# Performance work log

Hardware: AMD Instinct MI355X
Metric: run time of the kernel (lower is better)

The kernel has to match this reference:

```python
import jax, jax.numpy as jnp
import numpy as np

B, C, N, K = 2, 64, 16384, 16
C_OUT = 64


def setup_inputs() -> dict:
    key = jax.random.key(0)
    k1, k2, k3, k4 = jax.random.split(key, 4)
    x = jax.random.normal(k1, (B, C, N), dtype=jnp.float32)
    edge_index = jax.random.randint(k2, (2, B, N, K), 0, N, dtype=jnp.int64)
    # 1x1 Conv2d params: weight [C_out, 3C], bias [C_out]
    W = jax.random.normal(k3, (C_OUT, 3 * C), dtype=jnp.float32) * (1.0 / np.sqrt(3 * C))
    b = jax.random.normal(k4, (C_OUT,), dtype=jnp.float32) * 0.01
    return {"x": x, "edge_index": edge_index, "W": W, "b": b}


def _gather_nodes(x, idx):
    # x: [B, C, N], idx: [B, N, K] -> [B, C, N, K]
    return jax.vmap(lambda xb, ib: xb[:, ib])(x, idx)


def reference(x, edge_index, W, b):
    # x: [B, C, N]; edge_index: [2, B, N, K]
    x_i = _gather_nodes(x, edge_index[1])          # center features  [B,C,N,K]
    x_j = _gather_nodes(x, edge_index[0])          # neighbor features [B,C,N,K]
    edge_features = x_j - x_i                      # [B,C,N,K]
    global_feature = jnp.mean(x, axis=2, keepdims=True)  # [B,C,1] global mean over nodes
    global_rep = jnp.broadcast_to(global_feature[..., None], x_i.shape)  # [B,C,N,K]
    combined = jnp.concatenate([x_i, edge_features, global_rep], axis=1)  # [B,3C,N,K]
    # BasicConv: 1x1 conv + ReLU (norm=None)
    out = jnp.einsum("bcnk,oc->bonk", combined, W) + b[None, :, None, None]
    out = jax.nn.relu(out)
    return jnp.max(out, axis=-1, keepdims=True)    # [B,C_out,N,1]
```

## Files before the change

### kernel.cpp

```cpp
#include <hip/hip_runtime.h>
#include <hip/hip_bf16.h>


#define NNODES 16384
#define NCH 64

typedef _Float16 half8 __attribute__((ext_vector_type(8)));
typedef float f32x2 __attribute__((ext_vector_type(2)));

__global__ __launch_bounds__(256) void uv_kernel(const float* __restrict__ x,
                                                 const float* __restrict__ W,
                                                 _Float16* __restrict__ u,
                                                 _Float16* __restrict__ v,
                                                 float* __restrict__ g_slots) {
  __shared__ float A[64][64];
  __shared__ float Bm[64][64];
  __shared__ float csum[4][64];
  int t = threadIdx.x;
  {
    int o = t & 63, c0 = (t >> 6) * 16;
    const float* wr = W + o * 192;
#pragma unroll
    for (int i = 0; i < 16; ++i) {
      int c = c0 + i;
      float w1 = wr[c], w2 = wr[64 + c];
      A[c][o] = w1 - w2;
      Bm[c][o] = w2;
    }
  }
  __syncthreads();
  int lane = t & 63;
  int wv = __builtin_amdgcn_readfirstlane(t >> 6);
  int blk = blockIdx.x;
  int b = blk >> 9;
  int mb = (blk & 511) * 32;
  int m0 = mb + wv * 8;
  const float* xb = x + (size_t)b * (NCH * NNODES) + m0;
  f32x2 aU[4], aV[4];
#pragma unroll
  for (int i = 0; i < 4; ++i) {
    aU[i] = (f32x2){0.f, 0.f};
    aV[i] = (f32x2){0.f, 0.f};
  }
#pragma unroll 8
  for (int c = 0; c < 64; ++c) {
    float a = A[c][lane];
    float bb = Bm[c][lane];
    f32x2 a2 = {a, a};
    f32x2 b2 = {bb, bb};
    const float4* xr = (const float4*)(xb + (size_t)c * NNODES);
    float4 q0 = xr[0];
    float4 q1 = xr[1];
    f32x2 p0 = {q0.x, q0.y};
    f32x2 p1 = {q0.z, q0.w};
    f32x2 p2 = {q1.x, q1.y};
    f32x2 p3 = {q1.z, q1.w};
    aU[0] = __builtin_elementwise_fma(a2, p0, aU[0]);
    aU[1] = __builtin_elementwise_fma(a2, p1, aU[1]);
    aU[2] = __builtin_elementwise_fma(a2, p2, aU[2]);
    aU[3] = __builtin_elementwise_fma(a2, p3, aU[3]);
    aV[0] = __builtin_elementwise_fma(b2, p0, aV[0]);
    aV[1] = __builtin_elementwise_fma(b2, p1, aV[1]);
    aV[2] = __builtin_elementwise_fma(b2, p2, aV[2]);
    aV[3] = __builtin_elementwise_fma(b2, p3, aV[3]);
  }
  _Float16* ub = u + ((size_t)b * NNODES + m0) * NCH + lane;
  _Float16* vb = v + ((size_t)b * NNODES + m0) * NCH + lane;
#pragma unroll
  for (int i = 0; i < 4; ++i) {
    ub[(2 * i) * NCH] = (_Float16)aU[i][0];
    ub[(2 * i + 1) * NCH] = (_Float16)aU[i][1];
    vb[(2 * i) * NCH] = (_Float16)aV[i][0];
    vb[(2 * i + 1) * NCH] = (_Float16)aV[i][1];
  }
  {
    int c = t & 63, piece = t >> 6;
    const float4* xr2 =
        (const float4*)(x + (size_t)b * (NCH * NNODES) + (size_t)c * NNODES + mb + piece * 8);
    float4 a0 = xr2[0];
    float4 a1 = xr2[1];
    csum[piece][c] = ((a0.x + a0.y) + (a0.z + a0.w)) + ((a1.x + a1.y) + (a1.z + a1.w));
  }
  __syncthreads();
  if (t < 64) {
    float s = (csum[0][t] + csum[1][t]) + (csum[2][t] + csum[3][t]);
    atomicAdd(&g_slots[((blk & 7) << 7) + b * 64 + t], s);
  }
}

__global__ __launch_bounds__(256) void gather_kernel(const int* __restrict__ ei,
                                                     const _Float16* __restrict__ u,
                                                     const _Float16* __restrict__ v,
                                                     const float* __restrict__ W,
                                                     const float* __restrict__ bias,
                                                     const float* __restrict__ g_slots,
                                                     float* __restrict__ out) {
  __shared__ float tile[64][33];
  __shared__ float gb[64];
  __shared__ float pg[4][64];
  __shared__ float G_s[64];
  int t = threadIdx.x;
  int lane = t & 63;
  int wv = t >> 6;
  int blk = blockIdx.x;
  int xcd = blk & 7;
  int b = xcd >> 2;
  int nb = (blk >> 3) * 4 + (xcd & 3);
  int n0 = nb * 32;
  int q = lane >> 3;
  int r = lane & 7;
  const int* e0b = ei + (size_t)b * NNODES * 16;
  const int* e1b = ei + (size_t)(2 + b) * NNODES * 16;
  int f0 = (n0 + wv * 8) * 16 + q * 16 + r;
  int i0a = e0b[f0];
  int i0b = e0b[f0 + 8];
  int i1a = e1b[f0];
  int i1b = e1b[f0 + 8];
  if (t < 64) {
    float s = 0.f;
#pragma unroll
    for (int sl = 0; sl < 8; ++sl) s += g_slots[sl * 128 + b * 64 + t];
    gb[t] = s * (1.0f / 16384.0f);
  }
  __syncthreads();
  {
    int o = t >> 2, cq = t & 3;
    const float4* wr = (const float4*)(W + o * 192 + 128 + cq * 16);
    const float4* gr = (const float4*)(gb + cq * 16);
    float s = 0.f;
#pragma unroll
    for (int j = 0; j < 4; ++j) {
      float4 w = wr[j];
      float4 gg = gr[j];
      s += w.x * gg.x + w.y * gg.y + w.z * gg.z + w.w * gg.w;
    }
    pg[cq][o] = s;
  }
  __syncthreads();
  if (t < 64) G_s[t] = bias[t] + ((pg[0][t] + pg[1][t]) + (pg[2][t] + pg[3][t]));
  __syncthreads();
  const half8* u8 = (const half8*)(u + (size_t)b * NNODES * NCH) + r;
  const half8* v8 = (const half8*)(v + (size_t)b * NNODES * NCH) + r;
  half8 acc;
#pragma unroll
  for (int j = 0; j < 8; ++j) acc[j] = (_Float16)(-60000.0f);
#pragma unroll
  for (int k = 0; k < 16; ++k) {
    int src = (lane & 56) + (k & 7);
    int m1 = __shfl(k < 8 ? i1a : i1b, src, 64);
    int m0 = __shfl(k < 8 ? i0a : i0b, src, 64);
    half8 a = u8[(size_t)m1 * 8];
    half8 bb = v8[(size_t)m0 * 8];
    half8 s = a + bb;
    acc = __builtin_elementwise_max(acc, s);
  }
  int col = wv * 8 + q;
#pragma unroll
  for (int j = 0; j < 8; ++j) {
    tile[r * 8 + j][col] = fmaxf((float)acc[j] + G_s[r * 8 + j], 0.0f);
  }
  __syncthreads();
#pragma unroll
  for (int j = 0; j < 8; ++j) {
    int o = (t >> 5) + j * 8;
    int c2 = t & 31;
    out[((size_t)b * 64 + o) * NNODES + n0 + c2] = tile[o][c2];
  }
}

extern "C" void kernel_launch(void* const* d_in, const int* in_sizes, int n_in,
                              void* d_out, int out_size, void* d_ws, size_t ws_size,
                              hipStream_t stream) {
  const float* x = (const float*)d_in[0];
  const int* ei = (const int*)d_in[1];
  const float* W = (const float*)d_in[2];
  const float* bias = (const float*)d_in[3];
  float* out = (float*)d_out;

  char* ws = (char*)d_ws;
  _Float16* u = (_Float16*)ws;
  _Float16* v = (_Float16*)(ws + (size_t)4 * 1024 * 1024);
  float* g_slots = (float*)(ws + (size_t)8 * 1024 * 1024);

  hipMemsetAsync(g_slots, 0, 8 * 128 * sizeof(float), stream);
  uv_kernel<<<1024, 256, 0, stream>>>(x, W, u, v, g_slots);
  gather_kernel<<<1024, 256, 0, stream>>>(ei, u, v, W, bias, g_slots, out);
}
```

Before: 91.40 us.

## Precompute weight diff in prep kernel, stage x tile in LDS, batch gather loads

A small prep kernel now builds the interleaved (W1-W2, W2) matrix and zeroes the global-sum slots, which replaces the memset and the per-block weight transform. uv_kernel stages a 64x64 tile of x in LDS and computes column sums from that tile, so x is read from global memory once per block instead of twice. It also doubles the nodes per block and halves the grid. The gather loop issues 8 indexed loads before combining them, with two max accumulators and 32-bit offset math, to expose more memory-level parallelism. The cost is an extra kernel launch, more LDS per uv block and fewer uv blocks.

```diff
diff --git a/kernel.cpp b/kernel.cpp
--- a/kernel.cpp
+++ b/kernel.cpp
@@ -1,5 +1,4 @@
 #include <hip/hip_runtime.h>
-#include <hip/hip_bf16.h>
 
 
 #define NNODES 16384
@@ -8,83 +7,106 @@
 typedef _Float16 half8 __attribute__((ext_vector_type(8)));
 typedef float f32x2 __attribute__((ext_vector_type(2)));
 
+__global__ __launch_bounds__(64) void prep_kernel(const float* __restrict__ W,
+                                                  float2* __restrict__ ABg,
+                                                  float* __restrict__ g_slots) {
+  int o = blockIdx.x;
+  int t = threadIdx.x;
+  if (o == 0) {
+#pragma unroll
+    for (int i = 0; i < 16; ++i) g_slots[t + i * 64] = 0.0f;
+  }
+  float w1 = W[o * 192 + t];
+  float w2 = W[o * 192 + 64 + t];
+  ABg[t * 64 + o] = make_float2(w1 - w2, w2);
+}
+
 __global__ __launch_bounds__(256) void uv_kernel(const float* __restrict__ x,
-                                                 const float* __restrict__ W,
+                                                 const float2* __restrict__ ABg,
                                                  _Float16* __restrict__ u,
                                                  _Float16* __restrict__ v,
                                                  float* __restrict__ g_slots) {
-  __shared__ float A[64][64];
-  __shared__ float Bm[64][64];
-  __shared__ float csum[4][64];
+  __shared__ float2 ABs[64 * 64];
+  __shared__ float xs[64][64];
+  __shared__ float csumS[64];
   int t = threadIdx.x;
-  {
-    int o = t & 63, c0 = (t >> 6) * 16;
-    const float* wr = W + o * 192;
-#pragma unroll
-    for (int i = 0; i < 16; ++i) {
-      int c = c0 + i;
-      float w1 = wr[c], w2 = wr[64 + c];
-      A[c][o] = w1 - w2;
-      Bm[c][o] = w2;
-    }
-  }
-  __syncthreads();
   int lane = t & 63;
   int wv = __builtin_amdgcn_readfirstlane(t >> 6);
   int blk = blockIdx.x;
-  int b = blk >> 9;
-  int mb = (blk & 511) * 32;
-  int m0 = mb + wv * 8;
-  const float* xb = x + (size_t)b * (NCH * NNODES) + m0;
-  f32x2 aU[4], aV[4];
-#pragma unroll
-  for (int i = 0; i < 4; ++i) {
+  int b = blk >> 8;
+  int mb = (blk & 255) * 64;
+
+  {
+    const float4* src = (const float4*)ABg;
+    float4* dst = (float4*)ABs;
+#pragma unroll
+    for (int j = 0; j < 8; ++j) dst[t + j * 256] = src[t + j * 256];
+  }
+  {
+    const float* xb = x + (size_t)b * (NCH * NNODES) + mb;
+    int off = t & 15;
+#pragma unroll
+    for (int j = 0; j < 4; ++j) {
+      int c = (t >> 4) + j * 16;
+      float4 q = *(const float4*)(xb + (size_t)c * NNODES + off * 4);
+      *(float4*)&xs[c][off * 4] = q;
+      float s = (q.x + q.y) + (q.z + q.w);
+      s += __shfl_xor(s, 1, 16);
+      s += __shfl_xor(s, 2, 16);
+      s += __shfl_xor(s, 4, 16);
+      s += __shfl_xor(s, 8, 16);
+      if (off == 0) csumS[c] = s;
+    }
+  }
+  __syncthreads();
+  if (t < 64) atomicAdd(&g_slots[((blk & 7) << 7) + b * 64 + t], csumS[t]);
+
+  int m0 = wv * 16;
+  f32x2 aU[8], aV[8];
+#pragma unroll
+  for (int i = 0; i < 8; ++i) {
     aU[i] = (f32x2){0.f, 0.f};
     aV[i] = (f32x2){0.f, 0.f};
   }
 #pragma unroll 8
   for (int c = 0; c < 64; ++c) {
-    float a = A[c][lane];
-    float bb = Bm[c][lane];
-    f32x2 a2 = {a, a};
-    f32x2 b2 = {bb, bb};
-    const float4* xr = (const float4*)(xb + (size_t)c * NNODES);
+    float2 ab = ABs[c * 64 + lane];
+    f32x2 a2 = {ab.x, ab.x};
+    f32x2 b2 = {ab.y, ab.y};
+    const float4* xr = (const float4*)&xs[c][m0];
     float4 q0 = xr[0];
     float4 q1 = xr[1];
-    f32x2 p0 = {q0.x, q0.y};
-    f32x2 p1 = {q0.z, q0.w};
-    f32x2 p2 = {q1.x, q1.y};
-    f32x2 p3 = {q1.z, q1.w};
+    float4 q2 = xr[2];
+    float4 q3 = xr[3];
+    f32x2 p0 = {q0.x, q0.y}, p1 = {q0.z, q0.w};
+    f32x2 p2 = {q1.x, q1.y}, p3 = {q1.z, q1.w};
+    f32x2 p4 = {q2.x, q2.y}, p5 = {q2.z, q2.w};
+    f32x2 p6 = {q3.x, q3.y}, p7 = {q3.z, q3.w};
     aU[0] = __builtin_elementwise_fma(a2, p0, aU[0]);
     aU[1] = __builtin_elementwise_fma(a2, p1, aU[1]);
     aU[2] = __builtin_elementwise_fma(a2, p2, aU[2]);
     aU[3] = __builtin_elementwise_fma(a2, p3, aU[3]);
+    aU[4] = __builtin_elementwise_fma(a2, p4, aU[4]);
+    aU[5] = __builtin_elementwise_fma(a2, p5, aU[5]);
+    aU[6] = __builtin_elementwise_fma(a2, p6, aU[6]);
+    aU[7] = __builtin_elementwise_fma(a2, p7, aU[7]);
     aV[0] = __builtin_elementwise_fma(b2, p0, aV[0]);
     aV[1] = __builtin_elementwise_fma(b2, p1, aV[1]);
     aV[2] = __builtin_elementwise_fma(b2, p2, aV[2]);
     aV[3] = __builtin_elementwise_fma(b2, p3, aV[3]);
-  }
-  _Float16* ub = u + ((size_t)b * NNODES + m0) * NCH + lane;
-  _Float16* vb = v + ((size_t)b * NNODES + m0) * NCH + lane;
-#pragma unroll
-  for (int i = 0; i < 4; ++i) {
+    aV[4] = __builtin_elementwise_fma(b2, p4, aV[4]);
+    aV[5] = __builtin_elementwise_fma(b2, p5, aV[5]);
+    aV[6] = __builtin_elementwise_fma(b2, p6, aV[6]);
+    aV[7] = __builtin_elementwise_fma(b2, p7, aV[7]);
+  }
+  _Float16* ub = u + ((size_t)b * NNODES + mb + m0) * NCH + lane;
+  _Float16* vb = v + ((size_t)b * NNODES + mb + m0) * NCH + lane;
+#pragma unroll
+  for (int i = 0; i < 8; ++i) {
     ub[(2 * i) * NCH] = (_Float16)aU[i][0];
     ub[(2 * i + 1) * NCH] = (_Float16)aU[i][1];
     vb[(2 * i) * NCH] = (_Float16)aV[i][0];
     vb[(2 * i + 1) * NCH] = (_Float16)aV[i][1];
-  }
-  {
-    int c = t & 63, piece = t >> 6;
-    const float4* xr2 =
-        (const float4*)(x + (size_t)b * (NCH * NNODES) + (size_t)c * NNODES + mb + piece * 8);
-    float4 a0 = xr2[0];
-    float4 a1 = xr2[1];
-    csum[piece][c] = ((a0.x + a0.y) + (a0.z + a0.w)) + ((a1.x + a1.y) + (a1.z + a1.w));
-  }
-  __syncthreads();
-  if (t < 64) {
-    float s = (csum[0][t] + csum[1][t]) + (csum[2][t] + csum[3][t]);
-    atomicAdd(&g_slots[((blk & 7) << 7) + b * 64 + t], s);
   }
 }
 
@@ -139,21 +161,36 @@
   __syncthreads();
   if (t < 64) G_s[t] = bias[t] + ((pg[0][t] + pg[1][t]) + (pg[2][t] + pg[3][t]));
   __syncthreads();
-  const half8* u8 = (const half8*)(u + (size_t)b * NNODES * NCH) + r;
-  const half8* v8 = (const half8*)(v + (size_t)b * NNODES * NCH) + r;
-  half8 acc;
-#pragma unroll
-  for (int j = 0; j < 8; ++j) acc[j] = (_Float16)(-60000.0f);
-#pragma unroll
-  for (int k = 0; k < 16; ++k) {
-    int src = (lane & 56) + (k & 7);
-    int m1 = __shfl(k < 8 ? i1a : i1b, src, 64);
-    int m0 = __shfl(k < 8 ? i0a : i0b, src, 64);
-    half8 a = u8[(size_t)m1 * 8];
-    half8 bb = v8[(size_t)m0 * 8];
-    half8 s = a + bb;
-    acc = __builtin_elementwise_max(acc, s);
-  }
+  const char* ubase = (const char*)(u + (size_t)b * NNODES * NCH);
+  const char* vbase = (const char*)(v + (size_t)b * NNODES * NCH);
+  uint32_t r16 = (uint32_t)(r * 16);
+  half8 accA, accB;
+#pragma unroll
+  for (int j = 0; j < 8; ++j) {
+    accA[j] = (_Float16)(-60000.0f);
+    accB[j] = (_Float16)(-60000.0f);
+  }
+#pragma unroll
+  for (int h = 0; h < 2; ++h) {
+    half8 ua[8], va[8];
+#pragma unroll
+    for (int k = 0; k < 8; ++k) {
+      int src = (lane & 56) + k;
+      int m1 = __shfl(h ? i1b : i1a, src, 64);
+      int m0i = __shfl(h ? i0b : i0a, src, 64);
+      ua[k] = *(const half8*)(ubase + ((uint32_t)m1 * 128u + r16));
+      va[k] = *(const half8*)(vbase + ((uint32_t)m0i * 128u + r16));
+    }
+#pragma unroll
+    for (int k = 0; k < 8; ++k) {
+      half8 s = ua[k] + va[k];
+      if (k & 1)
+        accB = __builtin_elementwise_max(accB, s);
+      else
+        accA = __builtin_elementwise_max(accA, s);
+    }
+  }
+  half8 acc = __builtin_elementwise_max(accA, accB);
   int col = wv * 8 + q;
 #pragma unroll
   for (int j = 0; j < 8; ++j) {
@@ -181,8 +218,9 @@
   _Float16* u = (_Float16*)ws;
   _Float16* v = (_Float16*)(ws + (size_t)4 * 1024 * 1024);
   float* g_slots = (float*)(ws + (size_t)8 * 1024 * 1024);
-
-  hipMemsetAsync(g_slots, 0, 8 * 128 * sizeof(float), stream);
-  uv_kernel<<<1024, 256, 0, stream>>>(x, W, u, v, g_slots);
+  float2* ABg = (float2*)(ws + (size_t)8 * 1024 * 1024 + 4096);
+
+  prep_kernel<<<64, 64, 0, stream>>>(W, ABg, g_slots);
+  uv_kernel<<<512, 256, 0, stream>>>(x, ABg, u, v, g_slots);
   gather_kernel<<<1024, 256, 0, stream>>>(ei, u, v, W, bias, g_slots, out);
 }
```

Result: no change. 90.57 us (-0.9%).
